# Performance work log

Hardware: AMD Instinct MI355X
Metric: run time of the kernel (lower is better)

Reference implementation:

```python
import jax, jax.numpy as jnp
import numpy as np

B, T, D = 16, 4096, 768          # batch, tokens, hidden
N_BOX = 1024                      # total boxes across batch
MAX_BBOX = 128                    # cfg.MODEL.MAX_BBOX_NUM
DIM_DETR = 256                    # DETR feature dim (features[:,1:])


def _lin(k, din, dout):
    kw, kb = jax.random.split(k)
    s = 1.0 / np.sqrt(din)
    W = jax.random.uniform(kw, (dout, din), minval=-s, maxval=s, dtype=jnp.float32)
    b = jax.random.uniform(kb, (dout,), minval=-s, maxval=s, dtype=jnp.float32)
    return W, b


def setup_inputs() -> dict:
    key = jax.random.key(0)
    ks = jax.random.split(key, 10)
    inputs = jax.random.normal(ks[0], (B, T, D), dtype=jnp.float32)
    img = jnp.sort(jax.random.randint(ks[1], (N_BOX,), 0, B))
    rest = jax.random.randint(ks[2], (N_BOX, 4), 0, 224)
    bboxes = jnp.concatenate([img[:, None], rest], axis=1).astype(jnp.int32)
    features = jax.random.normal(ks[3], (N_BOX, 1 + DIM_DETR), dtype=jnp.float32)
    t1w, t1b = _lin(ks[4], D, D)      # transform layer 1
    t2w, t2b = _lin(ks[5], D, D)      # transform layer 2
    d1w, d1b = _lin(ks[6], D, D)      # deep_trans layer 1
    d2w, d2b = _lin(ks[7], D, D)      # deep_trans layer 2
    k8a, k8b = jax.random.split(ks[8])
    m1w, m1b = _lin(k8a, DIM_DETR, D) # mlp layer 1 (256->768)
    m2w, m2b = _lin(k8b, D, D)        # mlp layer 2
    pw, pb = _lin(ks[9], 2 * D, D)    # projection (1536->768)
    return dict(inputs=inputs, bboxes=bboxes, features=features,
                t1w=t1w, t1b=t1b, t2w=t2w, t2b=t2b,
                d1w=d1w, d1b=d1b, d2w=d2w, d2b=d2b,
                m1w=m1w, m1b=m1b, m2w=m2w, m2b=m2b,
                pw=pw, pb=pb)


def reference(inputs, bboxes, features, t1w, t1b, t2w, t2b,
              d1w, d1b, d2w, d2b, m1w, m1b, m2w, m2b, pw, pb):
    x = inputs.mean(axis=1)                                    # [B, D]
    ret_x = jax.nn.relu(x @ d1w.T + d1b) @ d2w.T + d2b         # deep_trans
    xt = jax.nn.relu(x @ t1w.T + t1b) @ t2w.T + t2b            # transform
    img = bboxes[:, 0]                                          # [N] image idx per box
    x_boxes = xt[img]                                           # broadcast image feat to its boxes
    fm = jax.nn.relu(features[:, 1:] @ m1w.T + m1b) @ m2w.T + m2b  # DETR mlp
    h = jnp.concatenate([x_boxes, fm], axis=1) @ pw.T + pb      # [N, D]
    # ragged pad: scatter each box into slot (img, rank-within-image)
    counts = jax.ops.segment_sum(jnp.ones((N_BOX,), jnp.int32), img, num_segments=B)
    offsets = jnp.cumsum(counts) - counts                       # exclusive cumsum (boxes sorted by img)
    pos = jnp.arange(N_BOX) - offsets[img]
    vis_output = jnp.zeros((B, MAX_BBOX, D), h.dtype).at[img, pos].set(h)
    att_mask = (jnp.arange(MAX_BBOX)[None, :] < counts[:, None]).astype(jnp.float32)
    return vis_output, att_mask, ret_x
```

## Files before the change

### kernel.cpp

```cpp
#include <hip/hip_runtime.h>

#define B_ 16
#define T_ 4096
#define D_ 768
#define NBOX 1024
#define MAXBB 128
#define DDETR 256

typedef unsigned short u16;
typedef short bf16x8 __attribute__((ext_vector_type(8)));
typedef float f32x4 __attribute__((ext_vector_type(4)));

__device__ __forceinline__ void split_bf(float f, u16& h, u16& l) {
    unsigned u = __builtin_bit_cast(unsigned, f);
    unsigned r = u + 0x7fffu + ((u >> 16) & 1u);
    u16 hb = (u16)(r >> 16);
    float hf = __builtin_bit_cast(float, (unsigned)hb << 16);
    float lf = f - hf;
    unsigned ul = __builtin_bit_cast(unsigned, lf);
    unsigned rl = ul + 0x7fffu + ((ul >> 16) & 1u);
    h = hb; l = (u16)(rl >> 16);
}

struct WDesc { const float* src; u16* hi; u16* lo; int N; int K; int stride; int vec; };
struct WPack8 { WDesc d[8]; };

__global__ __launch_bounds__(256) void k_front(WPack8 ws,
                                               const float4* __restrict__ in4,
                                               float4* __restrict__ part4,
                                               const int* __restrict__ bboxes,
                                               int* __restrict__ cnt_g, int* __restrict__ off_g,
                                               float* __restrict__ att, f32x4* __restrict__ vis4) {
    int bx = blockIdx.x;
    int tid = threadIdx.x;
    if (bx < 1024) {
        if (tid >= 192) return;
        int b = bx >> 6, c = bx & 63;
        const float4* base = in4 + (size_t)b * (T_ * D_ / 4) + (size_t)c * (64 * D_ / 4);
        float4 s = {0.f, 0.f, 0.f, 0.f};
        #pragma unroll 4
        for (int r = 0; r < 64; ++r) {
            float4 v = base[(size_t)r * 192 + tid];
            s.x += v.x; s.y += v.y; s.z += v.z; s.w += v.w;
        }
        part4[(size_t)bx * 192 + tid] = s;
        return;
    }
    if (bx < 2561) {
        int mb = bx - 1024;
        if (mb > 0) {
            int idx = (mb - 1) * 256 + tid;
            vis4[idx] = (f32x4){0.f, 0.f, 0.f, 0.f};
            return;
        }
        __shared__ int cnt[B_];
        __shared__ int off[B_];
        if (tid < B_) cnt[tid] = 0;
        __syncthreads();
        for (int i = tid; i < NBOX; i += 256) atomicAdd(&cnt[bboxes[i * 5]], 1);
        __syncthreads();
        if (tid == 0) {
            int acc = 0;
            for (int b = 0; b < B_; ++b) { off[b] = acc; acc += cnt[b]; }
        }
        __syncthreads();
        if (tid < B_) { cnt_g[tid] = cnt[tid]; off_g[tid] = off[tid]; }
        for (int j = tid; j < B_ * MAXBB; j += 256) {
            int b = j >> 7, p = j & 127;
            att[j] = (p < cnt[b]) ? 1.0f : 0.0f;
        }
        return;
    }
    int pidx = bx - 2561;
    WDesc d = ws.d[pidx / 576];
    int idx = (pidx % 576) * 256 + tid;
    int Kc = d.K >> 3;
    int total = d.N * Kc;
    if (idx >= total) return;
    int n = idx / Kc, kc = idx - n * Kc;
    const float* s = d.src + (size_t)n * d.stride + kc * 8;
    float v[8];
    if (d.vec) {
        f32x4 v0 = *(const f32x4*)s, v1 = *(const f32x4*)(s + 4);
        #pragma unroll
        for (int j = 0; j < 4; ++j) { v[j] = v0[j]; v[4 + j] = v1[j]; }
    } else {
        #pragma unroll
        for (int j = 0; j < 8; ++j) v[j] = s[j];
    }
    bf16x8 hv, lv;
    #pragma unroll
    for (int j = 0; j < 8; ++j) {
        u16 h, l;
        split_bf(v[j], h, l); hv[j] = (short)h; lv[j] = (short)l;
    }
    size_t off = ((size_t)(n >> 4) * Kc + kc) * 128 + (n & 15) * 8;
    *(bf16x8*)(d.hi + off) = hv;
    *(bf16x8*)(d.lo + off) = lv;
}

__global__ __launch_bounds__(256) void k_mean_final(const float* __restrict__ part,
                                                    u16* __restrict__ xph, u16* __restrict__ xpl) {
    __shared__ float xm[768];
    int b = blockIdx.x;
    int t = threadIdx.x;
    if (t < 192) {
        f32x4 s = {0.f, 0.f, 0.f, 0.f};
        #pragma unroll 4
        for (int c = 0; c < 64; ++c)
            s += *(const f32x4*)(part + ((size_t)(b * 64 + c)) * 768 + t * 4);
        s *= (1.0f / T_);
        *(f32x4*)(xm + t * 4) = s;
    }
    __syncthreads();
    if (t < 96) {
        const float* p = xm + t * 8;
        bf16x8 hv, lv;
        #pragma unroll
        for (int j = 0; j < 8; ++j) {
            u16 h, l;
            split_bf(p[j], h, l); hv[j] = (short)h; lv[j] = (short)l;
        }
        size_t off = ((size_t)t * 16 + b) * 8;
        *(bf16x8*)(xph + off) = hv;
        *(bf16x8*)(xpl + off) = lv;
    }
}

template<int GATHER>
__device__ __forceinline__ void dev_mfma(const u16* __restrict__ Ahi, const u16* __restrict__ Alo,
                                         const u16* __restrict__ Whi, const u16* __restrict__ Wlo,
                                         const u16* __restrict__ Xth, const u16* __restrict__ Xtl,
                                         const int* __restrict__ bbx,
                                         float* __restrict__ P, int Kc,
                                         int bxn, int byn, int term, int tid) {
    int lane = tid & 63, w = tid >> 6;
    int wm = w >> 1, wn = w & 1;
    int mt0 = byn * 8 + wm * 4;
    int nt0 = bxn * 8 + wn * 4;
    int nk = Kc >> 2;

    const u16* W = (term == 1) ? Wlo : Whi;
    const u16* Wp = W + ((size_t)nt0 * Kc) * 128 + lane * 8;
    size_t wstr = (size_t)Kc * 128;

    const u16* Ab = (term == 2) ? Alo : Ahi;
    const u16* Xb = (term == 2) ? Xtl : Xth;
    int AKc = GATHER ? 96 : Kc;
    size_t aofs[4], xofs[4];
    #pragma unroll
    for (int i = 0; i < 4; ++i)
        aofs[i] = ((size_t)(mt0 + i) * AKc) * 128 + lane * 8;
    if (GATHER) {
        #pragma unroll
        for (int i = 0; i < 4; ++i) {
            int row = (mt0 + i) * 16 + (lane & 15);
            xofs[i] = (size_t)(lane >> 4) * 128 + (size_t)bbx[row * 5] * 8;
        }
    }

    auto LA = [&](int k, bf16x8 (&a)[4]) {
        if (GATHER && k < 24) {
            #pragma unroll
            for (int i = 0; i < 4; ++i)
                a[i] = *(const bf16x8*)(Xb + xofs[i] + (size_t)k * 512);
        } else {
            int kk = GATHER ? k - 24 : k;
            #pragma unroll
            for (int i = 0; i < 4; ++i)
                a[i] = *(const bf16x8*)(Ab + aofs[i] + (size_t)kk * 512);
        }
    };

    bf16x8 a[4], b[4];
    LA(0, a);
    #pragma unroll
    for (int i = 0; i < 4; ++i) b[i] = *(const bf16x8*)(Wp + i * wstr);

    f32x4 acc[16];
    #pragma unroll
    for (int i = 0; i < 16; ++i) acc[i] = (f32x4){0.f, 0.f, 0.f, 0.f};

    for (int k = 0; k < nk; ++k) {
        bf16x8 an[4], bn[4];
        if (k + 1 < nk) {
            LA(k + 1, an);
            #pragma unroll
            for (int i = 0; i < 4; ++i)
                bn[i] = *(const bf16x8*)(Wp + i * wstr + (size_t)(k + 1) * 512);
        }
        #pragma unroll
        for (int i = 0; i < 4; ++i)
            #pragma unroll
            for (int j = 0; j < 4; ++j)
                acc[i * 4 + j] = __builtin_amdgcn_mfma_f32_16x16x32_bf16(a[i], b[j], acc[i * 4 + j], 0, 0, 0);
        #pragma unroll
        for (int i = 0; i < 4; ++i) { a[i] = an[i]; b[i] = bn[i]; }
    }

    float* Pz = P + (size_t)term * (1024 * 768);
    int rb = (lane >> 4) * 4, cb = lane & 15;
    #pragma unroll
    for (int i = 0; i < 4; ++i)
        #pragma unroll
        for (int j = 0; j < 4; ++j) {
            int row = (mt0 + i) * 16 + rb;
            int col = (nt0 + j) * 16 + cb;
            float* p = Pz + (size_t)row * 768 + col;
            f32x4 v = acc[i * 4 + j];
            #pragma unroll
            for (int r = 0; r < 4; ++r) p[(size_t)r * 768] = v[r];
        }
}

__device__ __forceinline__ void dev_epi_pack(int blk, int tid, int relu,
                                             const float* __restrict__ P,
                                             const float* __restrict__ bias,
                                             u16* __restrict__ dhi, u16* __restrict__ dlo,
                                             int KcDst, int kcOff) {
    int idx = blk * 256 + tid;
    int m = idx / 96, kc = idx - m * 96;
    const float* p0 = P + (size_t)m * 768 + kc * 8;
    f32x4 s0 = *(const f32x4*)p0, s1 = *(const f32x4*)(p0 + 4);
    #pragma unroll
    for (int z = 1; z < 3; ++z) {
        const float* p = p0 + (size_t)z * (1024 * 768);
        s0 += *(const f32x4*)p; s1 += *(const f32x4*)(p + 4);
    }
    s0 += *(const f32x4*)(bias + kc * 8);
    s1 += *(const f32x4*)(bias + kc * 8 + 4);
    bf16x8 hv, lv;
    #pragma unroll
    for (int j = 0; j < 4; ++j) {
        float v0 = relu ? fmaxf(s0[j], 0.f) : s0[j];
        float v1 = relu ? fmaxf(s1[j], 0.f) : s1[j];
        u16 h, l;
        split_bf(v0, h, l); hv[j] = (short)h; lv[j] = (short)l;
        split_bf(v1, h, l); hv[4 + j] = (short)h; lv[4 + j] = (short)l;
    }
    size_t off = ((size_t)(m >> 4) * KcDst + kcOff + kc) * 128 + (m & 15) * 8;
    *(bf16x8*)(dhi + off) = hv;
    *(bf16x8*)(dlo + off) = lv;
}

__global__ __launch_bounds__(256) void k_epi_vis(const float* __restrict__ P,
                                                 const float* __restrict__ bias,
                                                 float* __restrict__ vis,
                                                 const int* __restrict__ bbx,
                                                 const int* __restrict__ off) {
    int idx = blockIdx.x * 256 + threadIdx.x;
    int m = idx / 192, c4 = idx - m * 192;
    size_t o = (size_t)m * 768 + c4 * 4;
    f32x4 s = *(const f32x4*)(P + o);
    #pragma unroll
    for (int z = 1; z < 3; ++z) s += *(const f32x4*)(P + (size_t)z * (1024 * 768) + o);
    s += *(const f32x4*)(bias + c4 * 4);
    int b = bbx[m * 5];
    int pp = m - off[b];
    if (pp < MAXBB)
        *(f32x4*)&vis[((size_t)(b * MAXBB + pp)) * 768 + c4 * 4] = s;
}

__device__ __forceinline__ void dev_small(int bxn, int z, int tid,
                                          const u16* __restrict__ A0h, const u16* __restrict__ A0l,
                                          const u16* __restrict__ A1h, const u16* __restrict__ A1l,
                                          const u16* __restrict__ W0h, const u16* __restrict__ W0l,
                                          const u16* __restrict__ W1h, const u16* __restrict__ W1l,
                                          float* __restrict__ Ps) {
    int term = z >> 2, ks = z & 3;
    int lane = tid & 63, w = tid >> 6;
    int nt0 = bxn * 16 + w * 4;
    int path = nt0 >= 48;
    int ntp = nt0 - path * 48;
    const u16* Ah = path ? A1h : A0h;
    const u16* Al = path ? A1l : A0l;
    const u16* Wh = path ? W1h : W0h;
    const u16* Wl = path ? W1l : W0l;
    const u16* A = (term == 2) ? Al : Ah;
    const u16* W = (term == 1) ? Wl : Wh;
    int kc0 = ks * 24;

    const u16* Ap = A + (size_t)kc0 * 128 + lane * 8;
    const u16* Wp = W + ((size_t)ntp * 96 + kc0) * 128 + lane * 8;

    f32x4 acc[4];
    #pragma unroll
    for (int i = 0; i < 4; ++i) acc[i] = (f32x4){0.f, 0.f, 0.f, 0.f};

    #pragma unroll
    for (int k = 0; k < 6; ++k) {
        bf16x8 a = *(const bf16x8*)(Ap + (size_t)k * 512);
        bf16x8 b[4];
        #pragma unroll
        for (int j = 0; j < 4; ++j)
            b[j] = *(const bf16x8*)(Wp + (size_t)j * 96 * 128 + (size_t)k * 512);
        #pragma unroll
        for (int j = 0; j < 4; ++j)
            acc[j] = __builtin_amdgcn_mfma_f32_16x16x32_bf16(a, b[j], acc[j], 0, 0, 0);
    }

    float* Pz = Ps + (size_t)z * (16 * 1536);
    int rb = (lane >> 4) * 4, cb = lane & 15;
    #pragma unroll
    for (int j = 0; j < 4; ++j) {
        int col = (nt0 + j) * 16 + cb;
        float* p = Pz + (size_t)rb * 1536 + col;
        f32x4 v = acc[j];
        #pragma unroll
        for (int r = 0; r < 4; ++r) p[(size_t)r * 1536] = v[r];
    }
}

__device__ __forceinline__ void dev_sepi1(int blk, int tid,
                                          const float* __restrict__ Ps,
                                          const float* __restrict__ d1b, const float* __restrict__ t1b,
                                          u16* __restrict__ xh, u16* __restrict__ xl) {
    int idx = blk * 256 + tid;
    int r = idx / 192, cc = idx - r * 192;
    size_t base = (size_t)r * 1536 + cc * 8;
    f32x4 s0 = {0,0,0,0}, s1 = {0,0,0,0};
    for (int z = 0; z < 12; ++z) {
        const float* p = Ps + (size_t)z * (16 * 1536) + base;
        s0 += *(const f32x4*)p; s1 += *(const f32x4*)(p + 4);
    }
    int path = cc >= 96;
    int ccp = cc - path * 96;
    const float* bias = (path ? t1b : d1b) + ccp * 8;
    s0 += *(const f32x4*)bias;
    s1 += *(const f32x4*)(bias + 4);
    bf16x8 hv, lv;
    #pragma unroll
    for (int j = 0; j < 4; ++j) {
        u16 h, l;
        split_bf(fmaxf(s0[j], 0.f), h, l); hv[j] = (short)h; lv[j] = (short)l;
        split_bf(fmaxf(s1[j], 0.f), h, l); hv[4 + j] = (short)h; lv[4 + j] = (short)l;
    }
    size_t off = (size_t)path * 12288 + (size_t)ccp * 128 + r * 8;
    *(bf16x8*)(xh + off) = hv;
    *(bf16x8*)(xl + off) = lv;
}

__device__ __forceinline__ void dev_sepi2(int blk, int tid,
                                          const float* __restrict__ Ps,
                                          const float* __restrict__ d2b, const float* __restrict__ t2b,
                                          float* __restrict__ retx,
                                          u16* __restrict__ xth, u16* __restrict__ xtl) {
    int idx = blk * 256 + tid;
    int r = idx / 192, cc = idx - r * 192;
    size_t base = (size_t)r * 1536 + cc * 8;
    f32x4 s0 = {0,0,0,0}, s1 = {0,0,0,0};
    for (int z = 0; z < 12; ++z) {
        const float* p = Ps + (size_t)z * (16 * 1536) + base;
        s0 += *(const f32x4*)p; s1 += *(const f32x4*)(p + 4);
    }
    int path = cc >= 96;
    int ccp = cc - path * 96;
    const float* bias = (path ? t2b : d2b) + ccp * 8;
    s0 += *(const f32x4*)bias;
    s1 += *(const f32x4*)(bias + 4);
    if (!path) {
        float* o = retx + (size_t)r * 768 + ccp * 8;
        *(f32x4*)o = s0;
        *(f32x4*)(o + 4) = s1;
    } else {
        bf16x8 hv, lv;
        #pragma unroll
        for (int j = 0; j < 4; ++j) {
            u16 h, l;
            split_bf(s0[j], h, l); hv[j] = (short)h; lv[j] = (short)l;
            split_bf(s1[j], h, l); hv[4 + j] = (short)h; lv[4 + j] = (short)l;
        }
        size_t off = (size_t)ccp * 128 + r * 8;
        *(bf16x8*)(xth + off) = hv;
        *(bf16x8*)(xtl + off) = lv;
    }
}

__global__ __launch_bounds__(256) void k_phaseA(const u16* xph, const u16* xpl,
                                                const u16* d1wh, const u16* d1wl,
                                                const u16* t1wh, const u16* t1wl,
                                                float* Ps,
                                                const u16* feah, const u16* feal,
                                                const u16* m1wh, const u16* m1wl,
                                                float* P) {
    int bx = blockIdx.x, tid = threadIdx.x;
    if (bx < 72) {
        dev_small(bx % 6, bx / 6, tid, xph, xpl, xph, xpl,
                  d1wh, d1wl, t1wh, t1wl, Ps);
    } else {
        int i = bx - 72;
        dev_mfma<0>(feah, feal, m1wh, m1wl, nullptr, nullptr, nullptr,
                    P, 32, i % 6, (i / 6) % 8, i / 48, tid);
    }
}

__global__ __launch_bounds__(256) void k_phaseB(const float* Ps,
                                                const float* d1b, const float* t1b,
                                                u16* xch, u16* xcl,
                                                const float* P, const float* m1b,
                                                u16* fm1h, u16* fm1l) {
    int bx = blockIdx.x, tid = threadIdx.x;
    if (bx < 12) dev_sepi1(bx, tid, Ps, d1b, t1b, xch, xcl);
    else dev_epi_pack(bx - 12, tid, 1, P, m1b, fm1h, fm1l, 96, 0);
}

__global__ __launch_bounds__(256) void k_phaseC(const u16* xch, const u16* xcl,
                                                const u16* d2wh, const u16* d2wl,
                                                const u16* t2wh, const u16* t2wl,
                                                float* Ps,
                                                const u16* fm1h, const u16* fm1l,
                                                const u16* m2wh, const u16* m2wl,
                                                float* P) {
    int bx = blockIdx.x, tid = threadIdx.x;
    if (bx < 72) {
        dev_small(bx % 6, bx / 6, tid, xch, xcl, xch + 12288, xcl + 12288,
                  d2wh, d2wl, t2wh, t2wl, Ps);
    } else {
        int i = bx - 72;
        dev_mfma<0>(fm1h, fm1l, m2wh, m2wl, nullptr, nullptr, nullptr,
                    P, 96, i % 6, (i / 6) % 8, i / 48, tid);
    }
}

__global__ __launch_bounds__(256) void k_phaseD(const float* Ps,
                                                const float* d2b, const float* t2b,
                                                float* retx, u16* xth, u16* xtl,
                                                const float* P, const float* m2b,
                                                u16* fmh, u16* fml) {
    int bx = blockIdx.x, tid = threadIdx.x;
    if (bx < 12) dev_sepi2(bx, tid, Ps, d2b, t2b, retx, xth, xtl);
    else dev_epi_pack(bx - 12, tid, 0, P, m2b, fmh, fml, 96, 0);
}

__global__ __launch_bounds__(256) void k_pw(const u16* fmh, const u16* fml,
                                            const u16* pwh, const u16* pwl,
                                            const u16* xth, const u16* xtl,
                                            const int* bbx, float* P) {
    int i = blockIdx.x, tid = threadIdx.x;
    dev_mfma<1>(fmh, fml, pwh, pwl, xth, xtl, bbx,
                P, 192, i % 6, (i / 6) % 8, i / 48, tid);
}

extern "C" void kernel_launch(void* const* d_in, const int* in_sizes, int n_in,
                              void* d_out, int out_size, void* d_ws, size_t ws_size,
                              hipStream_t stream) {
    const float* inputs   = (const float*)d_in[0];
    const int*   bboxes   = (const int*)d_in[1];
    const float* features = (const float*)d_in[2];
    const float* t1w = (const float*)d_in[3];
    const float* t1b = (const float*)d_in[4];
    const float* t2w = (const float*)d_in[5];
    const float* t2b = (const float*)d_in[6];
    const float* d1w = (const float*)d_in[7];
    const float* d1b = (const float*)d_in[8];
    const float* d2w = (const float*)d_in[9];
    const float* d2b = (const float*)d_in[10];
    const float* m1w = (const float*)d_in[11];
    const float* m1b = (const float*)d_in[12];
    const float* m2w = (const float*)d_in[13];
    const float* m2b = (const float*)d_in[14];
    const float* pw  = (const float*)d_in[15];
    const float* pb  = (const float*)d_in[16];

    float* out  = (float*)d_out;
    float* vis  = out;
    float* att  = out + 1572864;
    float* retx = out + 1574912;

    float* wsf  = (float*)d_ws;
    float* part = wsf;
    float* P    = wsf + 786432;
    float* Ps   = P + 3 * 786432;
    int*   cnt  = (int*)(Ps + 294912);
    int*   off  = cnt + 16;
    u16*   sb   = (u16*)(off + 48);

    u16* t1wh = sb;              u16* t1wl = t1wh + 589824;
    u16* t2wh = t1wl + 589824;   u16* t2wl = t2wh + 589824;
    u16* d1wh = t2wl + 589824;   u16* d1wl = d1wh + 589824;
    u16* d2wh = d1wl + 589824;   u16* d2wl = d2wh + 589824;
    u16* m1wh = d2wl + 589824;   u16* m1wl = m1wh + 196608;
    u16* m2wh = m1wl + 196608;   u16* m2wl = m2wh + 589824;
    u16* pwh  = m2wl + 589824;   u16* pwl  = pwh + 1179648;
    u16* feah = pwl + 1179648;   u16* feal = feah + 262144;
    u16* fm1h = feal + 262144;   u16* fm1l = fm1h + 786432;
    u16* fmh  = fm1l + 786432;   u16* fml  = fmh + 786432;
    u16* xph  = fml + 786432;    u16* xpl  = xph + 12288;
    u16* xch  = xpl + 12288;     u16* xcl  = xch + 24576;
    u16* xth  = xcl + 24576;     u16* xtl  = xth + 12288;

    WPack8 wp;
    wp.d[0] = {t1w, t1wh, t1wl, 768, 768, 768, 1};
    wp.d[1] = {t2w, t2wh, t2wl, 768, 768, 768, 1};
    wp.d[2] = {d1w, d1wh, d1wl, 768, 768, 768, 1};
    wp.d[3] = {d2w, d2wh, d2wl, 768, 768, 768, 1};
    wp.d[4] = {m1w, m1wh, m1wl, 768, 256, 256, 1};
    wp.d[5] = {m2w, m2wh, m2wl, 768, 768, 768, 1};
    wp.d[6] = {pw,  pwh,  pwl,  768, 1536, 1536, 1};
    wp.d[7] = {features + 1, feah, feal, 1024, 256, 257, 0};
    k_front<<<7169, 256, 0, stream>>>(wp, (const float4*)inputs, (float4*)part,
                                      bboxes, cnt, off, att, (f32x4*)vis);

    k_mean_final<<<16, 256, 0, stream>>>(part, xph, xpl);

    k_phaseA<<<216, 256, 0, stream>>>(xph, xpl, d1wh, d1wl, t1wh, t1wl, Ps,
                                      feah, feal, m1wh, m1wl, P);

    k_phaseB<<<396, 256, 0, stream>>>(Ps, d1b, t1b, xch, xcl, P, m1b, fm1h, fm1l);

    k_phaseC<<<216, 256, 0, stream>>>(xch, xcl, d2wh, d2wl, t2wh, t2wl, Ps,
                                      fm1h, fm1l, m2wh, m2wl, P);

    k_phaseD<<<396, 256, 0, stream>>>(Ps, d2b, t2b, retx, xth, xtl, P, m2b, fmh, fml);

    k_pw<<<144, 256, 0, stream>>>(fmh, fml, pwh, pwl, xth, xtl, bboxes, P);

    k_epi_vis<<<768, 256, 0, stream>>>(P, pb, vis, bboxes, off);
}
```

Before: 404.7 us.

## Fuse post-front kernel chain into one cooperative persistent kernel with grid syncs

Result: slower. 607.6 us (+50.1%).

```diff
diff --git a/kernel.cpp b/kernel.cpp
--- a/kernel.cpp
+++ b/kernel.cpp
@@ -1,4 +1,7 @@
 #include <hip/hip_runtime.h>
+#include <hip/hip_cooperative_groups.h>
+
+namespace cg = cooperative_groups;
 
 #define B_ 16
 #define T_ 4096
@@ -99,11 +102,9 @@
     *(bf16x8*)(d.lo + off) = lv;
 }
 
-__global__ __launch_bounds__(256) void k_mean_final(const float* __restrict__ part,
-                                                    u16* __restrict__ xph, u16* __restrict__ xpl) {
-    __shared__ float xm[768];
-    int b = blockIdx.x;
-    int t = threadIdx.x;
+__device__ __forceinline__ void dev_mean_final(int b, int t, const float* __restrict__ part,
+                                               u16* __restrict__ xph, u16* __restrict__ xpl,
+                                               float* xm) {
     if (t < 192) {
         f32x4 s = {0.f, 0.f, 0.f, 0.f};
         #pragma unroll 4
@@ -243,12 +244,13 @@
     *(bf16x8*)(dlo + off) = lv;
 }
 
-__global__ __launch_bounds__(256) void k_epi_vis(const float* __restrict__ P,
-                                                 const float* __restrict__ bias,
-                                                 float* __restrict__ vis,
-                                                 const int* __restrict__ bbx,
-                                                 const int* __restrict__ off) {
-    int idx = blockIdx.x * 256 + threadIdx.x;
+__device__ __forceinline__ void dev_epi_vis(int blk, int tid,
+                                            const float* __restrict__ P,
+                                            const float* __restrict__ bias,
+                                            float* __restrict__ vis,
+                                            const int* __restrict__ bbx,
+                                            const int* __restrict__ off) {
+    int idx = blk * 256 + tid;
     int m = idx / 192, c4 = idx - m * 192;
     size_t o = (size_t)m * 768 + c4 * 4;
     f32x4 s = *(const f32x4*)(P + o);
@@ -376,69 +378,69 @@
     }
 }
 
-__global__ __launch_bounds__(256) void k_phaseA(const u16* xph, const u16* xpl,
-                                                const u16* d1wh, const u16* d1wl,
-                                                const u16* t1wh, const u16* t1wl,
-                                                float* Ps,
-                                                const u16* feah, const u16* feal,
-                                                const u16* m1wh, const u16* m1wl,
-                                                float* P) {
+struct ChainArgs {
+    const float* part;
+    float* P; float* Ps;
+    u16 *xph, *xpl, *xch, *xcl, *xth, *xtl;
+    const u16 *feah, *feal;
+    u16 *fm1h, *fm1l, *fmh, *fml;
+    const u16 *d1wh, *d1wl, *t1wh, *t1wl, *d2wh, *d2wl, *t2wh, *t2wl;
+    const u16 *m1wh, *m1wl, *m2wh, *m2wl, *pwh, *pwl;
+    const float *d1b, *t1b, *d2b, *t2b, *m1b, *m2b, *pb;
+    float* retx; float* vis;
+    const int* bbx; const int* off;
+};
+
+__global__ __launch_bounds__(256) void k_chain(ChainArgs A) {
+    cg::grid_group grid = cg::this_grid();
     int bx = blockIdx.x, tid = threadIdx.x;
-    if (bx < 72) {
-        dev_small(bx % 6, bx / 6, tid, xph, xpl, xph, xpl,
-                  d1wh, d1wl, t1wh, t1wl, Ps);
-    } else {
-        int i = bx - 72;
-        dev_mfma<0>(feah, feal, m1wh, m1wl, nullptr, nullptr, nullptr,
-                    P, 32, i % 6, (i / 6) % 8, i / 48, tid);
-    }
-}
-
-__global__ __launch_bounds__(256) void k_phaseB(const float* Ps,
-                                                const float* d1b, const float* t1b,
-                                                u16* xch, u16* xcl,
-                                                const float* P, const float* m1b,
-                                                u16* fm1h, u16* fm1l) {
-    int bx = blockIdx.x, tid = threadIdx.x;
-    if (bx < 12) dev_sepi1(bx, tid, Ps, d1b, t1b, xch, xcl);
-    else dev_epi_pack(bx - 12, tid, 1, P, m1b, fm1h, fm1l, 96, 0);
-}
-
-__global__ __launch_bounds__(256) void k_phaseC(const u16* xch, const u16* xcl,
-                                                const u16* d2wh, const u16* d2wl,
-                                                const u16* t2wh, const u16* t2wl,
-                                                float* Ps,
-                                                const u16* fm1h, const u16* fm1l,
-                                                const u16* m2wh, const u16* m2wl,
-                                                float* P) {
-    int bx = blockIdx.x, tid = threadIdx.x;
-    if (bx < 72) {
-        dev_small(bx % 6, bx / 6, tid, xch, xcl, xch + 12288, xcl + 12288,
-                  d2wh, d2wl, t2wh, t2wl, Ps);
-    } else {
-        int i = bx - 72;
-        dev_mfma<0>(fm1h, fm1l, m2wh, m2wl, nullptr, nullptr, nullptr,
-                    P, 96, i % 6, (i / 6) % 8, i / 48, tid);
-    }
-}
-
-__global__ __launch_bounds__(256) void k_phaseD(const float* Ps,
-                                                const float* d2b, const float* t2b,
-                                                float* retx, u16* xth, u16* xtl,
-                                                const float* P, const float* m2b,
-                                                u16* fmh, u16* fml) {
-    int bx = blockIdx.x, tid = threadIdx.x;
-    if (bx < 12) dev_sepi2(bx, tid, Ps, d2b, t2b, retx, xth, xtl);
-    else dev_epi_pack(bx - 12, tid, 0, P, m2b, fmh, fml, 96, 0);
-}
-
-__global__ __launch_bounds__(256) void k_pw(const u16* fmh, const u16* fml,
-                                            const u16* pwh, const u16* pwl,
-                                            const u16* xth, const u16* xtl,
-                                            const int* bbx, float* P) {
-    int i = blockIdx.x, tid = threadIdx.x;
-    dev_mfma<1>(fmh, fml, pwh, pwl, xth, xtl, bbx,
-                P, 192, i % 6, (i / 6) % 8, i / 48, tid);
+    __shared__ float xm[768];
+
+    if (bx < 16) {
+        dev_mean_final(bx, tid, A.part, A.xph, A.xpl, xm);
+    } else if (bx < 160) {
+        int i = bx - 16;
+        dev_mfma<0>(A.feah, A.feal, A.m1wh, A.m1wl, nullptr, nullptr, nullptr,
+                    A.P, 32, i % 6, (i / 6) % 8, i / 48, tid);
+    }
+    grid.sync();
+
+    if (bx < 72)
+        dev_small(bx % 6, bx / 6, tid, A.xph, A.xpl, A.xph, A.xpl,
+                  A.d1wh, A.d1wl, A.t1wh, A.t1wl, A.Ps);
+    for (int u = bx; u < 384; u += 256)
+        dev_epi_pack(u, tid, 1, A.P, A.m1b, A.fm1h, A.fm1l, 96, 0);
+    grid.sync();
+
+    if (bx < 12) {
+        dev_sepi1(bx, tid, A.Ps, A.d1b, A.t1b, A.xch, A.xcl);
+    } else if (bx >= 16 && bx < 160) {
+        int i = bx - 16;
+        dev_mfma<0>(A.fm1h, A.fm1l, A.m2wh, A.m2wl, nullptr, nullptr, nullptr,
+                    A.P, 96, i % 6, (i / 6) % 8, i / 48, tid);
+    }
+    grid.sync();
+
+    if (bx < 72)
+        dev_small(bx % 6, bx / 6, tid, A.xch, A.xcl, A.xch + 12288, A.xcl + 12288,
+                  A.d2wh, A.d2wl, A.t2wh, A.t2wl, A.Ps);
+    for (int u = bx; u < 384; u += 256)
+        dev_epi_pack(u, tid, 0, A.P, A.m2b, A.fmh, A.fml, 96, 0);
+    grid.sync();
+
+    if (bx < 12)
+        dev_sepi2(bx, tid, A.Ps, A.d2b, A.t2b, A.retx, A.xth, A.xtl);
+    grid.sync();
+
+    if (bx >= 16 && bx < 160) {
+        int i = bx - 16;
+        dev_mfma<1>(A.fmh, A.fml, A.pwh, A.pwl, A.xth, A.xtl, A.bbx,
+                    A.P, 192, i % 6, (i / 6) % 8, i / 48, tid);
+    }
+    grid.sync();
+
+    for (int u = bx; u < 768; u += 256)
+        dev_epi_vis(u, tid, A.P, A.pb, A.vis, A.bbx, A.off);
 }
 
 extern "C" void kernel_launch(void* const* d_in, const int* in_sizes, int n_in,
@@ -501,19 +503,20 @@
     k_front<<<7169, 256, 0, stream>>>(wp, (const float4*)inputs, (float4*)part,
                                       bboxes, cnt, off, att, (f32x4*)vis);
 
-    k_mean_final<<<16, 256, 0, stream>>>(part, xph, xpl);
-
-    k_phaseA<<<216, 256, 0, stream>>>(xph, xpl, d1wh, d1wl, t1wh, t1wl, Ps,
-                                      feah, feal, m1wh, m1wl, P);
-
-    k_phaseB<<<396, 256, 0, stream>>>(Ps, d1b, t1b, xch, xcl, P, m1b, fm1h, fm1l);
-
-    k_phaseC<<<216, 256, 0, stream>>>(xch, xcl, d2wh, d2wl, t2wh, t2wl, Ps,
-                                      fm1h, fm1l, m2wh, m2wl, P);
-
-    k_phaseD<<<396, 256, 0, stream>>>(Ps, d2b, t2b, retx, xth, xtl, P, m2b, fmh, fml);
-
-    k_pw<<<144, 256, 0, stream>>>(fmh, fml, pwh, pwl, xth, xtl, bboxes, P);
-
-    k_epi_vis<<<768, 256, 0, stream>>>(P, pb, vis, bboxes, off);
-}
+    ChainArgs ca;
+    ca.part = part; ca.P = P; ca.Ps = Ps;
+    ca.xph = xph; ca.xpl = xpl; ca.xch = xch; ca.xcl = xcl; ca.xth = xth; ca.xtl = xtl;
+    ca.feah = feah; ca.feal = feal;
+    ca.fm1h = fm1h; ca.fm1l = fm1l; ca.fmh = fmh; ca.fml = fml;
+    ca.d1wh = d1wh; ca.d1wl = d1wl; ca.t1wh = t1wh; ca.t1wl = t1wl;
+    ca.d2wh = d2wh; ca.d2wl = d2wl; ca.t2wh = t2wh; ca.t2wl = t2wl;
+    ca.m1wh = m1wh; ca.m1wl = m1wl; ca.m2wh = m2wh; ca.m2wl = m2wl;
+    ca.pwh = pwh; ca.pwl = pwl;
+    ca.d1b = d1b; ca.t1b = t1b; ca.d2b = d2b; ca.t2b = t2b;
+    ca.m1b = m1b; ca.m2b = m2b; ca.pb = pb;
+    ca.retx = retx; ca.vis = vis;
+    ca.bbx = bboxes; ca.off = off;
+
+    void* args[] = { &ca };
+    hipLaunchCooperativeKernel(k_chain, dim3(256), dim3(256), args, 0, stream);
+}
```

## Tile weight split-pack via LDS transpose and reschedule small-path phases across kernels

Applied to the files above, without the earlier changes.

Result: faster. 394.0 us (-2.7%).

```diff
diff --git a/kernel.cpp b/kernel.cpp
--- a/kernel.cpp
+++ b/kernel.cpp
@@ -31,6 +31,8 @@
                                                const int* __restrict__ bboxes,
                                                int* __restrict__ cnt_g, int* __restrict__ off_g,
                                                float* __restrict__ att, f32x4* __restrict__ vis4) {
+    __shared__ bf16x8 lh[16][17];
+    __shared__ bf16x8 ll[16][17];
     int bx = blockIdx.x;
     int tid = threadIdx.x;
     if (bx < 1024) {
@@ -72,13 +74,18 @@
         return;
     }
     int pidx = bx - 2561;
-    WDesc d = ws.d[pidx / 576];
-    int idx = (pidx % 576) * 256 + tid;
+    const int dEnd[8] = {288, 576, 864, 1152, 1248, 1536, 2112, 2240};
+    int di = 0;
+    #pragma unroll
+    for (int q = 0; q < 7; ++q) di += (pidx >= dEnd[q]);
+    WDesc d = ws.d[di];
+    int lb = pidx - (di == 0 ? 0 : dEnd[di - 1]);
     int Kc = d.K >> 3;
-    int total = d.N * Kc;
-    if (idx >= total) return;
-    int n = idx / Kc, kc = idx - n * Kc;
-    const float* s = d.src + (size_t)n * d.stride + kc * 8;
+    int kg = Kc >> 4;
+    int nt = lb / kg, kgi = lb - nt * kg;
+    int n0 = nt * 16, kc0 = kgi * 16;
+    int n_i = tid >> 4, kc_i = tid & 15;
+    const float* s = d.src + (size_t)(n0 + n_i) * d.stride + (kc0 + kc_i) * 8;
     float v[8];
     if (d.vec) {
         f32x4 v0 = *(const f32x4*)s, v1 = *(const f32x4*)(s + 4);
@@ -94,16 +101,18 @@
         u16 h, l;
         split_bf(v[j], h, l); hv[j] = (short)h; lv[j] = (short)l;
     }
-    size_t off = ((size_t)(n >> 4) * Kc + kc) * 128 + (n & 15) * 8;
-    *(bf16x8*)(d.hi + off) = hv;
-    *(bf16x8*)(d.lo + off) = lv;
-}
-
-__global__ __launch_bounds__(256) void k_mean_final(const float* __restrict__ part,
-                                                    u16* __restrict__ xph, u16* __restrict__ xpl) {
-    __shared__ float xm[768];
-    int b = blockIdx.x;
-    int t = threadIdx.x;
+    lh[kc_i][n_i] = hv;
+    ll[kc_i][n_i] = lv;
+    __syncthreads();
+    int kc_o = tid >> 4, n_o = tid & 15;
+    size_t off = ((size_t)nt * Kc + kc0 + kc_o) * 128 + n_o * 8;
+    *(bf16x8*)(d.hi + off) = lh[kc_o][n_o];
+    *(bf16x8*)(d.lo + off) = ll[kc_o][n_o];
+}
+
+__device__ __forceinline__ void dev_mean_final(int b, int t, const float* __restrict__ part,
+                                               u16* __restrict__ xph, u16* __restrict__ xpl,
+                                               float* xm) {
     if (t < 192) {
         f32x4 s = {0.f, 0.f, 0.f, 0.f};
         #pragma unroll 4
@@ -376,60 +385,70 @@
     }
 }
 
-__global__ __launch_bounds__(256) void k_phaseA(const u16* xph, const u16* xpl,
+__global__ __launch_bounds__(256) void k_phaseA(const float* part,
+                                                u16* xph, u16* xpl,
+                                                const u16* feah, const u16* feal,
+                                                const u16* m1wh, const u16* m1wl,
+                                                float* P) {
+    __shared__ float xm[768];
+    int bx = blockIdx.x, tid = threadIdx.x;
+    if (bx < 16) {
+        dev_mean_final(bx, tid, part, xph, xpl, xm);
+    } else {
+        int i = bx - 16;
+        dev_mfma<0>(feah, feal, m1wh, m1wl, nullptr, nullptr, nullptr,
+                    P, 32, i % 6, (i / 6) % 8, i / 48, tid);
+    }
+}
+
+__global__ __launch_bounds__(256) void k_phaseB(const u16* xph, const u16* xpl,
                                                 const u16* d1wh, const u16* d1wl,
                                                 const u16* t1wh, const u16* t1wl,
                                                 float* Ps,
-                                                const u16* feah, const u16* feal,
-                                                const u16* m1wh, const u16* m1wl,
-                                                float* P) {
-    int bx = blockIdx.x, tid = threadIdx.x;
-    if (bx < 72) {
-        dev_small(bx % 6, bx / 6, tid, xph, xpl, xph, xpl,
-                  d1wh, d1wl, t1wh, t1wl, Ps);
-    } else {
-        int i = bx - 72;
-        dev_mfma<0>(feah, feal, m1wh, m1wl, nullptr, nullptr, nullptr,
-                    P, 32, i % 6, (i / 6) % 8, i / 48, tid);
-    }
-}
-
-__global__ __launch_bounds__(256) void k_phaseB(const float* Ps,
-                                                const float* d1b, const float* t1b,
-                                                u16* xch, u16* xcl,
                                                 const float* P, const float* m1b,
                                                 u16* fm1h, u16* fm1l) {
     int bx = blockIdx.x, tid = threadIdx.x;
-    if (bx < 12) dev_sepi1(bx, tid, Ps, d1b, t1b, xch, xcl);
-    else dev_epi_pack(bx - 12, tid, 1, P, m1b, fm1h, fm1l, 96, 0);
-}
-
-__global__ __launch_bounds__(256) void k_phaseC(const u16* xch, const u16* xcl,
-                                                const u16* d2wh, const u16* d2wl,
-                                                const u16* t2wh, const u16* t2wl,
-                                                float* Ps,
+    if (bx < 72)
+        dev_small(bx % 6, bx / 6, tid, xph, xpl, xph, xpl,
+                  d1wh, d1wl, t1wh, t1wl, Ps);
+    else
+        dev_epi_pack(bx - 72, tid, 1, P, m1b, fm1h, fm1l, 96, 0);
+}
+
+__global__ __launch_bounds__(256) void k_phaseC(const float* Ps,
+                                                const float* d1b, const float* t1b,
+                                                u16* xch, u16* xcl,
                                                 const u16* fm1h, const u16* fm1l,
                                                 const u16* m2wh, const u16* m2wl,
                                                 float* P) {
     int bx = blockIdx.x, tid = threadIdx.x;
-    if (bx < 72) {
-        dev_small(bx % 6, bx / 6, tid, xch, xcl, xch + 12288, xcl + 12288,
-                  d2wh, d2wl, t2wh, t2wl, Ps);
+    if (bx < 12) {
+        dev_sepi1(bx, tid, Ps, d1b, t1b, xch, xcl);
     } else {
-        int i = bx - 72;
+        int i = bx - 12;
         dev_mfma<0>(fm1h, fm1l, m2wh, m2wl, nullptr, nullptr, nullptr,
                     P, 96, i % 6, (i / 6) % 8, i / 48, tid);
     }
 }
 
-__global__ __launch_bounds__(256) void k_phaseD(const float* Ps,
-                                                const float* d2b, const float* t2b,
-                                                float* retx, u16* xth, u16* xtl,
+__global__ __launch_bounds__(256) void k_phaseD(const u16* xch, const u16* xcl,
+                                                const u16* d2wh, const u16* d2wl,
+                                                const u16* t2wh, const u16* t2wl,
+                                                float* Ps,
                                                 const float* P, const float* m2b,
                                                 u16* fmh, u16* fml) {
     int bx = blockIdx.x, tid = threadIdx.x;
-    if (bx < 12) dev_sepi2(bx, tid, Ps, d2b, t2b, retx, xth, xtl);
-    else dev_epi_pack(bx - 12, tid, 0, P, m2b, fmh, fml, 96, 0);
+    if (bx < 72)
+        dev_small(bx % 6, bx / 6, tid, xch, xcl, xch + 12288, xcl + 12288,
+                  d2wh, d2wl, t2wh, t2wl, Ps);
+    else
+        dev_epi_pack(bx - 72, tid, 0, P, m2b, fmh, fml, 96, 0);
+}
+
+__global__ __launch_bounds__(256) void k_phaseE(const float* Ps,
+                                                const float* d2b, const float* t2b,
+                                                float* retx, u16* xth, u16* xtl) {
+    dev_sepi2(blockIdx.x, threadIdx.x, Ps, d2b, t2b, retx, xth, xtl);
 }
 
 __global__ __launch_bounds__(256) void k_pw(const u16* fmh, const u16* fml,
@@ -498,20 +517,21 @@
     wp.d[5] = {m2w, m2wh, m2wl, 768, 768, 768, 1};
     wp.d[6] = {pw,  pwh,  pwl,  768, 1536, 1536, 1};
     wp.d[7] = {features + 1, feah, feal, 1024, 256, 257, 0};
-    k_front<<<7169, 256, 0, stream>>>(wp, (const float4*)inputs, (float4*)part,
+    k_front<<<4801, 256, 0, stream>>>(wp, (const float4*)inputs, (float4*)part,
                                       bboxes, cnt, off, att, (f32x4*)vis);
 
-    k_mean_final<<<16, 256, 0, stream>>>(part, xph, xpl);
-
-    k_phaseA<<<216, 256, 0, stream>>>(xph, xpl, d1wh, d1wl, t1wh, t1wl, Ps,
-                                      feah, feal, m1wh, m1wl, P);
-
-    k_phaseB<<<396, 256, 0, stream>>>(Ps, d1b, t1b, xch, xcl, P, m1b, fm1h, fm1l);
-
-    k_phaseC<<<216, 256, 0, stream>>>(xch, xcl, d2wh, d2wl, t2wh, t2wl, Ps,
+    k_phaseA<<<160, 256, 0, stream>>>(part, xph, xpl, feah, feal, m1wh, m1wl, P);
+
+    k_phaseB<<<456, 256, 0, stream>>>(xph, xpl, d1wh, d1wl, t1wh, t1wl, Ps,
+                                      P, m1b, fm1h, fm1l);
+
+    k_phaseC<<<156, 256, 0, stream>>>(Ps, d1b, t1b, xch, xcl,
                                       fm1h, fm1l, m2wh, m2wl, P);
 
-    k_phaseD<<<396, 256, 0, stream>>>(Ps, d2b, t2b, retx, xth, xtl, P, m2b, fmh, fml);
+    k_phaseD<<<456, 256, 0, stream>>>(xch, xcl, d2wh, d2wl, t2wh, t2wl, Ps,
+                                      P, m2b, fmh, fml);
+
+    k_phaseE<<<12, 256, 0, stream>>>(Ps, d2b, t2b, retx, xth, xtl);
 
     k_pw<<<144, 256, 0, stream>>>(fmh, fml, pwh, pwl, xth, xtl, bboxes, P);
 
```
